# Optimization experiments

Measured on AMD Instinct MI355X. Metric: run time of the kernel, lower is better.

Reference implementation:

```python
import jax, jax.numpy as jnp
import numpy as np

B, P, E, D, A, M, V, L = 128, 196, 2048, 512, 512, 512, 10000, 21


def setup_inputs() -> dict:
    key = jax.random.key(0)
    ks = jax.random.split(key, 24)
    s = 0.02
    encoder_out = jax.random.normal(ks[0], (B, P, E), jnp.float32)
    encoded_captions = jax.random.randint(ks[1], (B, L), 0, V)
    caption_lengths = jax.random.randint(ks[2], (B,), 2, L + 1).at[0].set(L)
    return {
        "encoder_out": encoder_out,
        "encoded_captions": encoded_captions,
        "caption_lengths": caption_lengths,
        "emb_table": jax.random.normal(ks[3], (V, M), jnp.float32) * s,
        "enc_att_w": jax.random.normal(ks[4], (E, A), jnp.float32) * s,
        "enc_att_b": jnp.zeros((A,), jnp.float32),
        "dec_att_w": jax.random.normal(ks[5], (D, A), jnp.float32) * s,
        "dec_att_b": jnp.zeros((A,), jnp.float32),
        "full_att_w": jax.random.normal(ks[6], (A,), jnp.float32) * s,
        "full_att_b": jnp.zeros((), jnp.float32),
        "init_h_w": jax.random.normal(ks[7], (E, D), jnp.float32) * s,
        "init_h_b": jnp.zeros((D,), jnp.float32),
        "init_c_w": jax.random.normal(ks[8], (E, D), jnp.float32) * s,
        "init_c_b": jnp.zeros((D,), jnp.float32),
        "f_beta_w": jax.random.normal(ks[9], (D, E), jnp.float32) * s,
        "f_beta_b": jnp.zeros((E,), jnp.float32),
        "lstm_w_ih": jax.random.normal(ks[10], (4 * D, M + E), jnp.float32) * s,
        "lstm_b_ih": jnp.zeros((4 * D,), jnp.float32),
        "lstm_w_hh": jax.random.normal(ks[11], (4 * D, D), jnp.float32) * s,
        "lstm_b_hh": jnp.zeros((4 * D,), jnp.float32),
        "fc_w": jax.random.normal(ks[12], (V, D), jnp.float32) * s,
        "fc_b": jnp.zeros((V,), jnp.float32),
    }


def reference(encoder_out, encoded_captions, caption_lengths, emb_table,
              enc_att_w, enc_att_b, dec_att_w, dec_att_b, full_att_w, full_att_b,
              init_h_w, init_h_b, init_c_w, init_c_b, f_beta_w, f_beta_b,
              lstm_w_ih, lstm_b_ih, lstm_w_hh, lstm_b_hh, fc_w, fc_b):
    # sort by caption length descending (as in torch)
    order = jnp.argsort(-caption_lengths)
    enc = encoder_out[order]                 # [B,P,E]
    caps = encoded_captions[order]           # [B,L]
    dec_len = caption_lengths[order] - 1     # [B]
    T = caps.shape[1] - 1

    emb_seq = emb_table[caps]                # [B,L,M]
    mean = enc.mean(axis=1)                  # [B,E]
    h0 = mean @ init_h_w + init_h_b
    c0 = mean @ init_c_w + init_c_b
    att1 = enc @ enc_att_w + enc_att_b       # [B,P,A] (hoisted: constant over t)

    def step(carry, t):
        h, c = carry
        att2 = h @ dec_att_w + dec_att_b                              # [B,A]
        e = jnp.einsum('bpa,a->bp', jax.nn.relu(att1 + att2[:, None, :]), full_att_w) + full_att_b
        alpha = jax.nn.softmax(e, axis=1)                             # [B,P]
        awe = jnp.einsum('bpe,bp->be', enc, alpha)                    # [B,E]
        gate = jax.nn.sigmoid(h @ f_beta_w + f_beta_b)                # [B,E]
        x = jnp.concatenate([emb_seq[:, t, :], gate * awe], axis=1)   # [B,M+E]
        g = x @ lstm_w_ih.T + lstm_b_ih + h @ lstm_w_hh.T + lstm_b_hh
        i, f, gg, o = jnp.split(g, 4, axis=1)
        c_new = jax.nn.sigmoid(f) * c + jax.nn.sigmoid(i) * jnp.tanh(gg)
        h_new = jax.nn.sigmoid(o) * jnp.tanh(c_new)
        pred = h_new @ fc_w.T + fc_b                                  # [B,V]
        active = (t < dec_len)[:, None]
        pred = jnp.where(active, pred, 0.0)
        alpha = jnp.where(active, alpha, 0.0)
        return (h_new, c_new), (pred, alpha)

    _, (preds, alphas) = jax.lax.scan(step, (h0, c0), jnp.arange(T))
    predictions = jnp.moveaxis(preds, 0, 1)   # [B,T,V]
    alphas = jnp.moveaxis(alphas, 0, 1)       # [B,T,P]
    return predictions, alphas
```

## Files before the change

kernel.cpp:

```cpp
#include <hip/hip_runtime.h>
#include <math.h>

#define B_ 128
#define P_ 196
#define E_ 2048
#define D_ 512
#define A_ 512
#define M_ 512
#define V_ 10000
#define L_ 21
#define T_ 20

#define NBLK_ 256
#define SLOTS_WORDS (NBLK_ * 16 + 16)

typedef __attribute__((ext_vector_type(8))) short bf16x8;
typedef __attribute__((ext_vector_type(4))) float f32x4;
typedef unsigned short ushort_t;

__global__ void order_kernel(const int* __restrict__ lens, const int* __restrict__ caps,
                             int* __restrict__ order, int* __restrict__ declen,
                             int* __restrict__ row_map, int* __restrict__ tok_rows,
                             unsigned* __restrict__ bar) {
  __shared__ int s_order[B_];
  int tid = threadIdx.x;
  for (int i = tid; i < SLOTS_WORDS; i += 256) bar[i] = 0u;
  if (tid < B_) {
    int li = lens[tid];
    int r = 0;
    for (int j = 0; j < B_; ++j) {
      int lj = lens[j];
      r += (lj > li) || (lj == li && j < tid);
    }
    s_order[r] = tid;
    declen[r] = li - 1;
  }
  __syncthreads();
  if (tid < B_) order[tid] = s_order[tid];
  for (int m = tid; m < B_ * P_; m += blockDim.x) {
    int b = m / P_, p = m - b * P_;
    row_map[m] = s_order[b] * P_ + p;
  }
  for (int i = tid; i < T_ * B_; i += blockDim.x) {
    int t = i >> 7, b = i & 127;
    tok_rows[i] = caps[s_order[b] * L_ + t];
  }
}

__global__ void mean_kernel(const float* __restrict__ enc, const int* __restrict__ order,
                            float* __restrict__ mean) {
  int b = blockIdx.y;
  int e = blockIdx.x * blockDim.x + threadIdx.x;
  int ob = order[b];
  const float* base = enc + (long long)ob * P_ * E_ + e;
  float s = 0.f;
  for (int p = 0; p < P_; ++p) s += base[(long long)p * E_];
  mean[b * E_ + e] = s * (1.0f / P_);
}

__device__ __forceinline__ unsigned f2bf_u(float f) {
  unsigned u = __float_as_uint(f);
  return (u + 0x7fffu + ((u >> 16) & 1u)) >> 16;
}
__device__ __forceinline__ float bf2f(ushort_t h) {
  return __uint_as_float(((unsigned)h) << 16);
}

__global__ void enc2bf_kernel(const float* __restrict__ enc, const int* __restrict__ row_map,
                              ushort_t* __restrict__ out) {
  int r = blockIdx.x;
  int row = row_map[r];
  const float* src = enc + (long long)row * E_ + threadIdx.x * 8;
  float4 v0 = ((const float4*)src)[0];
  float4 v1 = ((const float4*)src)[1];
  float f[8] = {v0.x, v0.y, v0.z, v0.w, v1.x, v1.y, v1.z, v1.w};
  unsigned h[8];
#pragma unroll
  for (int j = 0; j < 8; ++j) h[j] = f2bf_u(f[j]);
  int4 o;
  o.x = (int)(h[0] | (h[1] << 16));
  o.y = (int)(h[2] | (h[3] << 16));
  o.z = (int)(h[4] | (h[5] << 16));
  o.w = (int)(h[6] | (h[7] << 16));
  *(int4*)(out + (long long)r * E_ + threadIdx.x * 8) = o;
}

__global__ void transpose_kernel(const float* __restrict__ in, float* __restrict__ out,
                                 int K, int N) {
  __shared__ float tt[32][33];
  int bx = blockIdx.x * 32;
  int by = blockIdx.y * 32;
  int lx = threadIdx.x & 31, ly = threadIdx.x >> 5;
#pragma unroll
  for (int i = 0; i < 32; i += 8) tt[ly + i][lx] = in[(long long)(by + ly + i) * N + bx + lx];
  __syncthreads();
#pragma unroll
  for (int i = 0; i < 32; i += 8)
    out[(long long)(bx + ly + i) * K + by + lx] = tt[lx][ly + i];
}

__global__ __launch_bounds__(256) void gemm32_kernel(
    const float* __restrict__ A, const float* __restrict__ Bm,
    const float* __restrict__ bias, float* __restrict__ C, int M, int N, int K) {
  __shared__ float As[16][64];
  __shared__ float Bs[16][64];
  const int tid = threadIdx.x;
  const int bm = blockIdx.y * 64, bn = blockIdx.x * 64;
  const int tm = tid >> 4, tn = tid & 15;
  float acc[4][4];
#pragma unroll
  for (int i = 0; i < 4; ++i)
#pragma unroll
    for (int j = 0; j < 4; ++j) acc[i][j] = 0.f;
  const int lm = tid >> 2;
  const int lk = (tid & 3) * 4;
  for (int k0 = 0; k0 < K; k0 += 16) {
    {
      int m = bm + lm;
      float4 v = make_float4(0.f, 0.f, 0.f, 0.f);
      if (m < M) v = *(const float4*)(A + (long long)m * K + k0 + lk);
      As[lk + 0][lm] = v.x;
      As[lk + 1][lm] = v.y;
      As[lk + 2][lm] = v.z;
      As[lk + 3][lm] = v.w;
    }
    {
      int k = tid >> 4;
      int n4 = (tid & 15) * 4;
      int n = bn + n4;
      float4 v = make_float4(0.f, 0.f, 0.f, 0.f);
      if (n < N) v = *(const float4*)(Bm + (long long)(k0 + k) * N + n);
      Bs[k][n4 + 0] = v.x;
      Bs[k][n4 + 1] = v.y;
      Bs[k][n4 + 2] = v.z;
      Bs[k][n4 + 3] = v.w;
    }
    __syncthreads();
#pragma unroll
    for (int k = 0; k < 16; ++k) {
      float a0 = As[k][tm * 4 + 0], a1 = As[k][tm * 4 + 1];
      float a2 = As[k][tm * 4 + 2], a3 = As[k][tm * 4 + 3];
      float b0 = Bs[k][tn * 4 + 0], b1 = Bs[k][tn * 4 + 1];
      float b2 = Bs[k][tn * 4 + 2], b3 = Bs[k][tn * 4 + 3];
      acc[0][0] += a0 * b0; acc[0][1] += a0 * b1; acc[0][2] += a0 * b2; acc[0][3] += a0 * b3;
      acc[1][0] += a1 * b0; acc[1][1] += a1 * b1; acc[1][2] += a1 * b2; acc[1][3] += a1 * b3;
      acc[2][0] += a2 * b0; acc[2][1] += a2 * b1; acc[2][2] += a2 * b2; acc[2][3] += a2 * b3;
      acc[3][0] += a3 * b0; acc[3][1] += a3 * b1; acc[3][2] += a3 * b2; acc[3][3] += a3 * b3;
    }
    __syncthreads();
  }
#pragma unroll
  for (int i = 0; i < 4; ++i) {
    int m = bm + tm * 4 + i;
    if (m >= M) continue;
#pragma unroll
    for (int j = 0; j < 4; ++j) {
      int n = bn + tn * 4 + j;
      if (n >= N) continue;
      C[(long long)m * N + n] = acc[i][j] + (bias ? bias[n] : 0.f);
    }
  }
}

__device__ __forceinline__ void stage16(short* __restrict__ Ph, short* __restrict__ Pl,
                                        int r, int kq, float4 v0, float4 v1, float4 v2,
                                        float4 v3, bool split) {
  float f[16] = {v0.x, v0.y, v0.z, v0.w, v1.x, v1.y, v1.z, v1.w,
                 v2.x, v2.y, v2.z, v2.w, v3.x, v3.y, v3.z, v3.w};
#pragma unroll
  for (int g2 = 0; g2 < 2; ++g2) {
    int gg = (kq >> 3) + g2;
    int slot = gg ^ ((r >> 1) & 3);
    unsigned hb[8];
    float lf[8];
#pragma unroll
    for (int j = 0; j < 8; ++j) {
      float x = f[g2 * 8 + j];
      hb[j] = f2bf_u(x);
      lf[j] = x - __uint_as_float(hb[j] << 16);
    }
    int4 ph;
    ph.x = (int)(hb[0] | (hb[1] << 16));
    ph.y = (int)(hb[2] | (hb[3] << 16));
    ph.z = (int)(hb[4] | (hb[5] << 16));
    ph.w = (int)(hb[6] | (hb[7] << 16));
    *(int4*)&Ph[r * 32 + slot * 8] = ph;
    if (split) {
      unsigned lb[8];
#pragma unroll
      for (int j = 0; j < 8; ++j) lb[j] = f2bf_u(lf[j]);
      int4 pl;
      pl.x = (int)(lb[0] | (lb[1] << 16));
      pl.y = (int)(lb[2] | (lb[3] << 16));
      pl.z = (int)(lb[4] | (lb[5] << 16));
      pl.w = (int)(lb[6] | (lb[7] << 16));
      *(int4*)&Pl[r * 32 + slot * 8] = pl;
    }
  }
}

__device__ __forceinline__ void stage8(short* __restrict__ Ph, short* __restrict__ Pl,
                                       int r, int kq8, float4 v0, float4 v1) {
  int slot = kq8 ^ ((r >> 1) & 3);
  float f[8] = {v0.x, v0.y, v0.z, v0.w, v1.x, v1.y, v1.z, v1.w};
  unsigned hb[8];
  float lf[8];
#pragma unroll
  for (int j = 0; j < 8; ++j) {
    hb[j] = f2bf_u(f[j]);
    lf[j] = f[j] - __uint_as_float(hb[j] << 16);
  }
  int4 ph;
  ph.x = (int)(hb[0] | (hb[1] << 16));
  ph.y = (int)(hb[2] | (hb[3] << 16));
  ph.z = (int)(hb[4] | (hb[5] << 16));
  ph.w = (int)(hb[6] | (hb[7] << 16));
  *(int4*)&Ph[r * 32 + slot * 8] = ph;
  unsigned lb[8];
#pragma unroll
  for (int j = 0; j < 8; ++j) lb[j] = f2bf_u(lf[j]);
  int4 pl;
  pl.x = (int)(lb[0] | (lb[1] << 16));
  pl.y = (int)(lb[2] | (lb[3] << 16));
  pl.z = (int)(lb[4] | (lb[5] << 16));
  pl.w = (int)(lb[6] | (lb[7] << 16));
  *(int4*)&Pl[r * 32 + slot * 8] = pl;
}

__device__ __forceinline__ bf16x8 frag_load(const short* __restrict__ P, int row, int g) {
  int slot = g ^ ((row >> 1) & 3);
  return *(const bf16x8*)&P[row * 32 + slot * 8];
}

template <int MODE, bool SPLIT, bool SWZ, bool OB>
__global__ __launch_bounds__(256) void mfma_gemm(
    const float* __restrict__ A, int lda, const int* __restrict__ row_map,
    const float* __restrict__ Bn, int ldb,
    const float* __restrict__ bias, const float* __restrict__ bias2,
    void* __restrict__ Cv, int ldc, int M, int N, int K,
    const int* __restrict__ declen) {
  __shared__ short Ah[128 * 32];
  __shared__ short Bh[128 * 32];
  __shared__ short Al[128 * 32];
  __shared__ short Bl[128 * 32];
  const int tid = threadIdx.x;
  int bxi, byi;
  if (SWZ) {
    int gx = gridDim.x, gy = gridDim.y;
    int id = blockIdx.y * gx + blockIdx.x;
    int super = 8 * gx;
    int body = (gy & ~7) * gx;
    if (id < body) {
      int s = id / super, rem = id % super;
      byi = s * 8 + (rem & 7);
      bxi = rem >> 3;
    } else {
      int rem = id - body;
      byi = (gy & ~7) + rem / gx;
      bxi = rem % gx;
    }
  } else {
    bxi = blockIdx.x;
    byi = blockIdx.y;
  }
  const int bm = byi * 128, bn = bxi * 128;

  f32x4 acc[4][4];
#pragma unroll
  for (int i = 0; i < 4; ++i)
#pragma unroll
    for (int j = 0; j < 4; ++j) acc[i][j] = (f32x4){0.f, 0.f, 0.f, 0.f};

  const int r = tid >> 1;
  const int kq = (tid & 1) * 16;
  const int am = bm + r;
  const long long arow = row_map ? (long long)row_map[am] : (long long)am;
  const float* ap = A + arow * (long long)lda + kq;
  const int gn = bn + r;
  const float* bp = Bn + (long long)gn * ldb + kq;
  const bool bok = gn < N;

  const int lane = tid & 63;
  const int wv = tid >> 6, wr = wv >> 1, wc = wv & 1;
  const int lr = lane & 15, g = lane >> 4;

  float4 z4 = make_float4(0.f, 0.f, 0.f, 0.f);
  float4 a0 = *(const float4*)(ap), a1 = *(const float4*)(ap + 4);
  float4 a2 = *(const float4*)(ap + 8), a3 = *(const float4*)(ap + 12);
  float4 b0 = bok ? *(const float4*)(bp) : z4;
  float4 b1 = bok ? *(const float4*)(bp + 4) : z4;
  float4 b2 = bok ? *(const float4*)(bp + 8) : z4;
  float4 b3 = bok ? *(const float4*)(bp + 12) : z4;

  for (int k0 = 0; k0 < K; k0 += 32) {
    stage16(Ah, Al, r, kq, a0, a1, a2, a3, SPLIT);
    stage16(Bh, Bl, r, kq, b0, b1, b2, b3, SPLIT);
    __syncthreads();
    if (k0 + 32 < K) {
      int kn = k0 + 32;
      a0 = *(const float4*)(ap + kn);
      a1 = *(const float4*)(ap + kn + 4);
      a2 = *(const float4*)(ap + kn + 8);
      a3 = *(const float4*)(ap + kn + 12);
      b0 = bok ? *(const float4*)(bp + kn) : z4;
      b1 = bok ? *(const float4*)(bp + kn + 4) : z4;
      b2 = bok ? *(const float4*)(bp + kn + 8) : z4;
      b3 = bok ? *(const float4*)(bp + kn + 12) : z4;
    }
    bf16x8 ah[4], bh[4];
#pragma unroll
    for (int i = 0; i < 4; ++i) {
      ah[i] = frag_load(Ah, wr * 64 + i * 16 + lr, g);
      bh[i] = frag_load(Bh, wc * 64 + i * 16 + lr, g);
    }
#pragma unroll
    for (int i = 0; i < 4; ++i)
#pragma unroll
      for (int j = 0; j < 4; ++j)
        acc[i][j] = __builtin_amdgcn_mfma_f32_16x16x32_bf16(ah[i], bh[j], acc[i][j], 0, 0, 0);
    if (SPLIT) {
      bf16x8 al2[4], bl2[4];
#pragma unroll
      for (int i = 0; i < 4; ++i) {
        al2[i] = frag_load(Al, wr * 64 + i * 16 + lr, g);
        bl2[i] = frag_load(Bl, wc * 64 + i * 16 + lr, g);
      }
#pragma unroll
      for (int i = 0; i < 4; ++i)
#pragma unroll
        for (int j = 0; j < 4; ++j)
          acc[i][j] = __builtin_amdgcn_mfma_f32_16x16x32_bf16(al2[i], bh[j], acc[i][j], 0, 0, 0);
#pragma unroll
      for (int i = 0; i < 4; ++i)
#pragma unroll
        for (int j = 0; j < 4; ++j)
          acc[i][j] = __builtin_amdgcn_mfma_f32_16x16x32_bf16(ah[i], bl2[j], acc[i][j], 0, 0, 0);
    }
    __syncthreads();
  }

#pragma unroll
  for (int j = 0; j < 4; ++j) {
    int n = bn + wc * 64 + j * 16 + lr;
    float bj = 0.f;
    if (n < N) {
      if (bias) bj += bias[n];
      if (bias2) bj += bias2[n];
    }
#pragma unroll
    for (int i = 0; i < 4; ++i) {
#pragma unroll
      for (int rr = 0; rr < 4; ++rr) {
        int m = bm + wr * 64 + i * 16 + g * 4 + rr;
        float v = acc[i][j][rr] + bj;
        if (MODE == 0) {
          if (OB)
            ((ushort_t*)Cv)[(long long)m * ldc + n] = (ushort_t)f2bf_u(v);
          else
            ((float*)Cv)[(long long)m * ldc + n] = v;
        } else {
          if (n < N) {
            int b = m & 127, t = m >> 7;
            ((float*)Cv)[(long long)b * (T_ * V_) + (long long)t * V_ + n] =
                (t < declen[b]) ? v : 0.f;
          }
        }
      }
    }
  }
}

__device__ __forceinline__ void mfma_tile64(
    const float* __restrict__ ap, const float* __restrict__ bp, int K,
    f32x4 (&acc)[2][2], short* Ah, short* Al, short* Bh, short* Bl,
    int sr, int skq, int wr, int wc, int lr, int g) {
  float4 a0 = *(const float4*)(ap), a1 = *(const float4*)(ap + 4);
  float4 b0 = *(const float4*)(bp), b1 = *(const float4*)(bp + 4);
  for (int k0 = 0; k0 < K; k0 += 32) {
    stage8(Ah, Al, sr, skq, a0, a1);
    stage8(Bh, Bl, sr, skq, b0, b1);
    __syncthreads();
    if (k0 + 32 < K) {
      a0 = *(const float4*)(ap + k0 + 32);
      a1 = *(const float4*)(ap + k0 + 36);
      b0 = *(const float4*)(bp + k0 + 32);
      b1 = *(const float4*)(bp + k0 + 36);
    }
    bf16x8 fah[2], fbh[2], fal[2], fbl[2];
#pragma unroll
    for (int i = 0; i < 2; ++i) {
      fah[i] = frag_load(Ah, wr * 32 + i * 16 + lr, g);
      fal[i] = frag_load(Al, wr * 32 + i * 16 + lr, g);
      fbh[i] = frag_load(Bh, wc * 32 + i * 16 + lr, g);
      fbl[i] = frag_load(Bl, wc * 32 + i * 16 + lr, g);
    }
#pragma unroll
    for (int i = 0; i < 2; ++i)
#pragma unroll
      for (int j = 0; j < 2; ++j) {
        acc[i][j] = __builtin_amdgcn_mfma_f32_16x16x32_bf16(fah[i], fbh[j], acc[i][j], 0, 0, 0);
        acc[i][j] = __builtin_amdgcn_mfma_f32_16x16x32_bf16(fal[i], fbh[j], acc[i][j], 0, 0, 0);
        acc[i][j] = __builtin_amdgcn_mfma_f32_16x16x32_bf16(fah[i], fbl[j], acc[i][j], 0, 0, 0);
      }
    __syncthreads();
  }
}

__device__ __forceinline__ void gsync(unsigned* __restrict__ slots, unsigned target) {
  __syncthreads();
  if (threadIdx.x == 0) {
    __threadfence();
    __hip_atomic_store(&slots[blockIdx.x * 16], target, __ATOMIC_RELEASE,
                       __HIP_MEMORY_SCOPE_AGENT);
  }
  if (threadIdx.x < 64) {
#pragma unroll
    for (int k = 0; k < 4; ++k) {
      unsigned idx = ((unsigned)threadIdx.x * 4 + k) * 16;
      while (__hip_atomic_load(&slots[idx], __ATOMIC_ACQUIRE, __HIP_MEMORY_SCOPE_AGENT) <
             target) {
        __builtin_amdgcn_s_sleep(2);
      }
    }
    __threadfence();
  }
  __syncthreads();
}

template <bool ENCBF>
__global__ __launch_bounds__(256, 1) void loop_kernel(
    const float* __restrict__ att1f, const ushort_t* __restrict__ att1b,
    const float* __restrict__ encf, const ushort_t* __restrict__ encb,
    const int* __restrict__ order, const int* __restrict__ declen,
    const float* __restrict__ decT, const float* __restrict__ decb,
    const float* __restrict__ fbT, const float* __restrict__ fbb,
    const float* __restrict__ whh, const float* __restrict__ wih,
    const float* __restrict__ faw, const float* __restrict__ fab,
    const float* __restrict__ g_all, float* __restrict__ g_part,
    float* __restrict__ gh, float* __restrict__ h_all, float* __restrict__ c,
    float* __restrict__ xh, float* __restrict__ gate, float* __restrict__ att2,
    float* __restrict__ alphas_out, unsigned* __restrict__ bar) {
  __shared__ short Ah[64 * 32];
  __shared__ short Bh[64 * 32];
  __shared__ short Al[64 * 32];
  __shared__ short Bl[64 * 32];
  __shared__ float att2_s[512];
  __shared__ float w_s[512];
  __shared__ float e_s[P_];
  __shared__ float red[8];

  unsigned* slots = bar;
  unsigned tgt = 0;

  const int bid = blockIdx.x, tid = threadIdx.x;
  const int lane = tid & 63, wv = tid >> 6, wr = wv >> 1, wc = wv & 1;
  const int lr = lane & 15, g = lane >> 4;
  const int sr = tid >> 2, skq = tid & 3;

  const float fb0 = fab[0];
  float wr8[8];
  if (ENCBF) {
    const float4* wp = (const float4*)(faw + lane * 8);
#pragma unroll
    for (int q = 0; q < 2; ++q) {
      float4 v = wp[q];
      wr8[q * 4 + 0] = v.x;
      wr8[q * 4 + 1] = v.y;
      wr8[q * 4 + 2] = v.z;
      wr8[q * 4 + 3] = v.w;
    }
  }

  for (int t = 0; t < T_; ++t) {
    const float* h_cur = h_all + t * (B_ * D_);
    if (bid < 144) {
      int nt = bid % 72, mt = bid / 72;
      int bn = nt * 64;
      const float* Bb;
      if (bn < 512) Bb = decT + bn * 512;
      else if (bn < 2560) Bb = fbT + (bn - 512) * 512;
      else Bb = whh + (bn - 2560) * 512;
      f32x4 acc[2][2];
#pragma unroll
      for (int i = 0; i < 2; ++i)
#pragma unroll
        for (int j = 0; j < 2; ++j) acc[i][j] = (f32x4){0.f, 0.f, 0.f, 0.f};
      mfma_tile64(h_cur + (mt * 64 + sr) * 512 + skq * 8, Bb + sr * 512 + skq * 8, 512,
                  acc, Ah, Al, Bh, Bl, sr, skq, wr, wc, lr, g);
#pragma unroll
      for (int j = 0; j < 2; ++j) {
        int n = bn + wc * 32 + j * 16 + lr;
#pragma unroll
        for (int i = 0; i < 2; ++i) {
#pragma unroll
          for (int rr = 0; rr < 4; ++rr) {
            int m = mt * 64 + wr * 32 + i * 16 + g * 4 + rr;
            float v = acc[i][j][rr];
            if (bn < 512) {
              att2[m * 512 + n] = v + decb[n];
            } else if (bn < 2560) {
              int nc = n - 512;
              gate[m * 2048 + nc] = 1.f / (1.f + __expf(-(v + fbb[nc])));
            } else {
              gh[m * 2048 + (n - 2560)] = v;
            }
          }
        }
      }
    }
    gsync(slots, ++tgt);
    {
      const int b = bid & 127, half = bid >> 7;
      if (ENCBF) {
        float a2r[8];
        const float4* a2p = (const float4*)(att2 + b * 512 + lane * 8);
#pragma unroll
        for (int q = 0; q < 2; ++q) {
          float4 v = a2p[q];
          a2r[q * 4 + 0] = v.x;
          a2r[q * 4 + 1] = v.y;
          a2r[q * 4 + 2] = v.z;
          a2r[q * 4 + 3] = v.w;
        }
        for (int p = wv; p < P_; p += 4) {
          const ushort_t* row = att1b + ((long long)(b * P_ + p)) * 512 + lane * 8;
          bf16x8 hv = *(const bf16x8*)row;
          float s = 0.f;
#pragma unroll
          for (int j = 0; j < 8; ++j) {
            float x = bf2f((ushort_t)hv[j]) + a2r[j];
            s += (x > 0.f ? x : 0.f) * wr8[j];
          }
          for (int off = 32; off; off >>= 1) s += __shfl_down(s, off);
          if (lane == 0) e_s[p] = s + fb0;
        }
      } else {
        for (int i = tid; i < 512; i += 256) {
          att2_s[i] = att2[b * 512 + i];
          w_s[i] = faw[i];
        }
        __syncthreads();
        for (int p = wv; p < P_; p += 4) {
          const float* row = att1f + ((long long)b * P_ + p) * 512;
          float s = 0.f;
#pragma unroll
          for (int i2 = 0; i2 < 8; ++i2) {
            int ix = lane + i2 * 64;
            float v = row[ix] + att2_s[ix];
            s += (v > 0.f ? v : 0.f) * w_s[ix];
          }
          for (int off = 32; off; off >>= 1) s += __shfl_down(s, off);
          if (lane == 0) e_s[p] = s + fb0;
        }
      }
      __syncthreads();
      float mx = -1e30f;
      for (int p = tid; p < P_; p += 256) mx = fmaxf(mx, e_s[p]);
      for (int off = 32; off; off >>= 1) mx = fmaxf(mx, __shfl_down(mx, off));
      if (lane == 0) red[wv] = mx;
      __syncthreads();
      mx = fmaxf(fmaxf(red[0], red[1]), fmaxf(red[2], red[3]));
      float ssum = 0.f;
      for (int p = tid; p < P_; p += 256) {
        float ev = __expf(e_s[p] - mx);
        e_s[p] = ev;
        ssum += ev;
      }
      for (int off = 32; off; off >>= 1) ssum += __shfl_down(ssum, off);
      if (lane == 0) red[4 + wv] = ssum;
      __syncthreads();
      float inv = 1.f / (red[4] + red[5] + red[6] + red[7]);
      const bool active = (t < declen[b]);
      for (int p = tid; p < P_; p += 256) {
        float al = e_s[p] * inv;
        e_s[p] = al;
        if (half == 0)
          alphas_out[(long long)b * (T_ * P_) + t * P_ + p] = active ? al : 0.f;
      }
      __syncthreads();
      if (ENCBF) {
        const ushort_t* eb = encb + (long long)b * (P_ * E_);
        int col = half * 1024 + tid * 4;
        float s0 = 0.f, s1 = 0.f, s2 = 0.f, s3 = 0.f;
#pragma unroll 8
        for (int p = 0; p < P_; ++p) {
          short4 hv = *(const short4*)(eb + (long long)p * E_ + col);
          float a = e_s[p];
          s0 += a * bf2f((ushort_t)hv.x);
          s1 += a * bf2f((ushort_t)hv.y);
          s2 += a * bf2f((ushort_t)hv.z);
          s3 += a * bf2f((ushort_t)hv.w);
        }
        float4 gv = *(const float4*)(gate + b * 2048 + col);
        float4 o;
        o.x = gv.x * s0;
        o.y = gv.y * s1;
        o.z = gv.z * s2;
        o.w = gv.w * s3;
        *(float4*)(xh + b * 2048 + col) = o;
      } else {
        const int ob = order[b];
        const float* eb = encf + (long long)ob * (P_ * E_);
        for (int e0 = half * 1024 + tid; e0 < half * 1024 + 1024; e0 += 256) {
          float s2 = 0.f;
#pragma unroll 4
          for (int p = 0; p < P_; ++p) s2 += e_s[p] * eb[p * 2048 + e0];
          xh[b * 2048 + e0] = gate[b * 2048 + e0] * s2;
        }
      }
    }
    gsync(slots, ++tgt);
    {
      int kc = bid >> 6, rem = bid & 63, mt = rem >> 5, nt = rem & 31;
      int bn = nt * 64;
      f32x4 acc[2][2];
#pragma unroll
      for (int i = 0; i < 2; ++i)
#pragma unroll
        for (int j = 0; j < 2; ++j) acc[i][j] = (f32x4){0.f, 0.f, 0.f, 0.f};
      mfma_tile64(xh + (mt * 64 + sr) * 2048 + kc * 512 + skq * 8,
                  wih + (long long)(bn + sr) * 2560 + 512 + kc * 512 + skq * 8, 512,
                  acc, Ah, Al, Bh, Bl, sr, skq, wr, wc, lr, g);
      float* gp = g_part + kc * (128 * 2048);
#pragma unroll
      for (int j = 0; j < 2; ++j) {
        int n = bn + wc * 32 + j * 16 + lr;
#pragma unroll
        for (int i = 0; i < 2; ++i) {
#pragma unroll
          for (int rr = 0; rr < 4; ++rr) {
            int m = mt * 64 + wr * 32 + i * 16 + g * 4 + rr;
            gp[m * 2048 + n] = acc[i][j][rr];
          }
        }
      }
    }
    gsync(slots, ++tgt);
    {
      int idx = bid * 256 + tid;
      int b = idx >> 9, d = idx & 511;
      int base = b * 2048 + d;
      const float* ge = g_all + (long long)t * (128 * 2048);
      float gi = ge[base] + gh[base];
      float gf2 = ge[base + 512] + gh[base + 512];
      float gg2 = ge[base + 1024] + gh[base + 1024];
      float go = ge[base + 1536] + gh[base + 1536];
#pragma unroll
      for (int kc = 0; kc < 4; ++kc) {
        const float* gp = g_part + kc * (128 * 2048) + base;
        gi += gp[0];
        gf2 += gp[512];
        gg2 += gp[1024];
        go += gp[1536];
      }
      float si = 1.f / (1.f + __expf(-gi));
      float sf = 1.f / (1.f + __expf(-gf2));
      float so = 1.f / (1.f + __expf(-go));
      float cn = sf * c[idx] + si * tanhf(gg2);
      float hn = so * tanhf(cn);
      c[idx] = cn;
      h_all[(t + 1) * (B_ * D_) + idx] = hn;
    }
    gsync(slots, ++tgt);
  }
}

extern "C" void kernel_launch(void* const* d_in, const int* in_sizes, int n_in,
                              void* d_out, int out_size, void* d_ws, size_t ws_size,
                              hipStream_t stream) {
  const float* enc       = (const float*)d_in[0];
  const int*   caps      = (const int*)d_in[1];
  const int*   lens      = (const int*)d_in[2];
  const float* emb       = (const float*)d_in[3];
  const float* enc_att_w = (const float*)d_in[4];
  const float* enc_att_b = (const float*)d_in[5];
  const float* dec_att_w = (const float*)d_in[6];
  const float* dec_att_b = (const float*)d_in[7];
  const float* full_att_w = (const float*)d_in[8];
  const float* full_att_b = (const float*)d_in[9];
  const float* init_h_w  = (const float*)d_in[10];
  const float* init_h_b  = (const float*)d_in[11];
  const float* init_c_w  = (const float*)d_in[12];
  const float* init_c_b  = (const float*)d_in[13];
  const float* f_beta_w  = (const float*)d_in[14];
  const float* f_beta_b  = (const float*)d_in[15];
  const float* lstm_w_ih = (const float*)d_in[16];
  const float* lstm_b_ih = (const float*)d_in[17];
  const float* lstm_w_hh = (const float*)d_in[18];
  const float* lstm_b_hh = (const float*)d_in[19];
  const float* fc_w      = (const float*)d_in[20];
  const float* fc_b      = (const float*)d_in[21];

  float* out = (float*)d_out;
  float* alphas_out = out + (long long)B_ * T_ * V_;

  float* g_all    = out;
  float* g_part   = out + 6 * 1024 * 1024;
  float* encattwT = out + 8 * 1024 * 1024;
  float* decT     = out + 9 * 1024 * 1024 + 512 * 1024;
  float* fbT      = decT + 512 * 512;
  float* gh       = out + 12 * 1024 * 1024;

  size_t cur = 0;
  char* wsb = (char*)d_ws;
  auto alloc = [&](size_t bytes) {
    size_t off = cur;
    cur = (cur + bytes + 255) & ~(size_t)255;
    return (void*)(wsb + off);
  };
  const size_t ATT1B_BYTES = (size_t)B_ * P_ * A_ * 2;
  const size_t ENCB_BYTES  = (size_t)B_ * P_ * E_ * 2;
  const size_t ATT1F_BYTES = (size_t)B_ * P_ * A_ * 4;
  const size_t REST_BYTES  = (size_t)(B_ * E_ + (T_ + 1) * B_ * D_ + B_ * D_ + B_ * A_ +
                                      B_ * E_ + B_ * E_) * 4 +
                             (2 * B_ + B_ * P_ + T_ * B_ + SLOTS_WORDS + 64) * 4 + 4096;
  const bool bfpath = ws_size >= ATT1B_BYTES + ENCB_BYTES + REST_BYTES + (1u << 20);

  ushort_t* att1b = nullptr;
  ushort_t* encbf = nullptr;
  float* att1f = nullptr;
  if (bfpath) {
    att1b = (ushort_t*)alloc(ATT1B_BYTES);
    encbf = (ushort_t*)alloc(ENCB_BYTES);
  } else {
    att1f = (float*)alloc(ATT1F_BYTES);
  }
  float* mean  = (float*)alloc((size_t)B_ * E_ * 4);
  float* h_all = (float*)alloc((size_t)(T_ + 1) * B_ * D_ * 4);
  float* c     = (float*)alloc((size_t)B_ * D_ * 4);
  float* att2  = (float*)alloc((size_t)B_ * A_ * 4);
  float* gate  = (float*)alloc((size_t)B_ * E_ * 4);
  float* xh    = (float*)alloc((size_t)B_ * E_ * 4);
  int* order   = (int*)alloc(B_ * 4);
  int* declen  = (int*)alloc(B_ * 4);
  int* row_map = (int*)alloc((size_t)B_ * P_ * 4);
  int* tok_rows = (int*)alloc((size_t)T_ * B_ * 4);
  unsigned* bar = (unsigned*)alloc(SLOTS_WORDS * 4);

  hipLaunchKernelGGL(order_kernel, dim3(1), dim3(256), 0, stream, lens, caps, order, declen,
                     row_map, tok_rows, bar);
  hipLaunchKernelGGL(transpose_kernel, dim3(16, 64), dim3(256), 0, stream, enc_att_w,
                     encattwT, E_, A_);
  hipLaunchKernelGGL(transpose_kernel, dim3(16, 16), dim3(256), 0, stream, dec_att_w, decT,
                     D_, A_);
  hipLaunchKernelGGL(transpose_kernel, dim3(64, 16), dim3(256), 0, stream, f_beta_w, fbT,
                     D_, E_);
  hipLaunchKernelGGL(mean_kernel, dim3(E_ / 256, B_), dim3(256), 0, stream, enc, order, mean);
  hipLaunchKernelGGL(gemm32_kernel, dim3(D_ / 64, 2), dim3(256), 0, stream, mean, init_h_w,
                     init_h_b, h_all, B_, D_, E_);
  hipLaunchKernelGGL(gemm32_kernel, dim3(D_ / 64, 2), dim3(256), 0, stream, mean, init_c_w,
                     init_c_b, c, B_, D_, E_);
  if (bfpath) {
    hipLaunchKernelGGL((mfma_gemm<0, false, true, true>), dim3(A_ / 128, (B_ * P_) / 128),
                       dim3(256), 0, stream, enc, E_, row_map, encattwT, E_, enc_att_b,
                       (const float*)nullptr, (void*)att1b, A_, B_ * P_, A_, E_,
                       (const int*)nullptr);
    hipLaunchKernelGGL(enc2bf_kernel, dim3(B_ * P_), dim3(256), 0, stream, enc, row_map,
                       encbf);
  } else {
    hipLaunchKernelGGL((mfma_gemm<0, false, true, false>), dim3(A_ / 128, (B_ * P_) / 128),
                       dim3(256), 0, stream, enc, E_, row_map, encattwT, E_, enc_att_b,
                       (const float*)nullptr, (void*)att1f, A_, B_ * P_, A_, E_,
                       (const int*)nullptr);
  }
  hipLaunchKernelGGL((mfma_gemm<0, true, false, false>), dim3((4 * D_) / 128, (T_ * B_) / 128),
                     dim3(256), 0, stream, emb, M_, tok_rows, lstm_w_ih, M_ + E_, lstm_b_ih,
                     lstm_b_hh, (void*)g_all, 4 * D_, T_ * B_, 4 * D_, M_,
                     (const int*)nullptr);
  if (bfpath) {
    hipLaunchKernelGGL((loop_kernel<true>), dim3(NBLK_), dim3(256), 0, stream,
                       (const float*)nullptr, att1b, (const float*)nullptr, encbf, order,
                       declen, decT, dec_att_b, fbT, f_beta_b, lstm_w_hh, lstm_w_ih,
                       full_att_w, full_att_b, g_all, g_part, gh, h_all, c, xh, gate, att2,
                       alphas_out, bar);
  } else {
    hipLaunchKernelGGL((loop_kernel<false>), dim3(NBLK_), dim3(256), 0, stream, att1f,
                       (const ushort_t*)nullptr, enc, (const ushort_t*)nullptr, order,
                       declen, decT, dec_att_b, fbT, f_beta_b, lstm_w_hh, lstm_w_ih,
                       full_att_w, full_att_b, g_all, g_part, gh, h_all, c, xh, gate, att2,
                       alphas_out, bar);
  }
  hipLaunchKernelGGL((mfma_gemm<1, true, false, false>), dim3((V_ + 127) / 128,
                     (T_ * B_) / 128), dim3(256), 0, stream, h_all + B_ * D_, D_,
                     (const int*)nullptr, fc_w, D_, fc_b, (const float*)nullptr, (void*)out,
                     V_, T_ * B_, V_, D_, declen);
}
```

Measured before the change: 5.493 ms.

## Split attention score computation across block pairs and widen weighted-sum loads

In the bf16 path each batch row is handled by two blocks. Before, both blocks computed all 196 attention scores, duplicating the work. Now each block computes half of the scores with batched 8-row loads, publishes them to global memory, and exchanges them with its partner block through a pairwise acquire/release flag spin. The weighted encoder sum now uses 8-wide bf16 loads with a register prefetch pipeline, and the thread groups split the P dimension in halves, combining their partial sums through shared memory. This adds a partner synchronisation per step and a global round trip for scores, in return for halving the redundant score work and improving memory-level parallelism.

Result: faster. 5.261 ms (-4.2%).

```diff
diff --git a/kernel.cpp b/kernel.cpp
--- a/kernel.cpp
+++ b/kernel.cpp
@@ -12,7 +12,7 @@
 #define T_ 20
 
 #define NBLK_ 256
-#define SLOTS_WORDS (NBLK_ * 16 + 16)
+#define SLOTS_WORDS (NBLK_ * 16 + NBLK_ * 16 + 16)
 
 typedef __attribute__((ext_vector_type(8))) short bf16x8;
 typedef __attribute__((ext_vector_type(4))) float f32x4;
@@ -439,7 +439,8 @@
     const float* __restrict__ g_all, float* __restrict__ g_part,
     float* __restrict__ gh, float* __restrict__ h_all, float* __restrict__ c,
     float* __restrict__ xh, float* __restrict__ gate, float* __restrict__ att2,
-    float* __restrict__ alphas_out, unsigned* __restrict__ bar) {
+    float* __restrict__ alphas_out, unsigned* __restrict__ bar,
+    float* __restrict__ e_g) {
   __shared__ short Ah[64 * 32];
   __shared__ short Bh[64 * 32];
   __shared__ short Al[64 * 32];
@@ -450,6 +451,7 @@
   __shared__ float red[8];
 
   unsigned* slots = bar;
+  unsigned* pf = bar + NBLK_ * 16;
   unsigned tgt = 0;
 
   const int bid = blockIdx.x, tid = threadIdx.x;
@@ -522,18 +524,61 @@
           a2r[q * 4 + 2] = v.z;
           a2r[q * 4 + 3] = v.w;
         }
-        for (int p = wv; p < P_; p += 4) {
-          const ushort_t* row = att1b + ((long long)(b * P_ + p)) * 512 + lane * 8;
-          bf16x8 hv = *(const bf16x8*)row;
-          float s = 0.f;
-#pragma unroll
-          for (int j = 0; j < 8; ++j) {
-            float x = bf2f((ushort_t)hv[j]) + a2r[j];
-            s += (x > 0.f ? x : 0.f) * wr8[j];
+        const int pbase = half * 98;
+        const ushort_t* a1base = att1b + ((long long)b * P_ + pbase) * 512 + lane * 8;
+        const bf16x8 zv = (bf16x8)(short)0;
+        for (int p0 = wv * 8; p0 < 98; p0 += 32) {
+          bf16x8 hv[8];
+#pragma unroll
+          for (int q = 0; q < 8; ++q) {
+            int p = p0 + q;
+            hv[q] = (p < 98) ? *(const bf16x8*)(a1base + (long long)p * 512) : zv;
           }
-          for (int off = 32; off; off >>= 1) s += __shfl_down(s, off);
-          if (lane == 0) e_s[p] = s + fb0;
-        }
+          float s[8];
+#pragma unroll
+          for (int q = 0; q < 8; ++q) {
+            float sq = 0.f;
+#pragma unroll
+            for (int j = 0; j < 8; ++j) {
+              float x = bf2f((ushort_t)hv[q][j]) + a2r[j];
+              sq += (x > 0.f ? x : 0.f) * wr8[j];
+            }
+            s[q] = sq;
+          }
+#pragma unroll
+          for (int off = 32; off; off >>= 1) {
+#pragma unroll
+            for (int q = 0; q < 8; ++q) s[q] += __shfl_down(s[q], off);
+          }
+          if (lane == 0) {
+#pragma unroll
+            for (int q = 0; q < 8; ++q) {
+              int p = p0 + q;
+              if (p < 98) {
+                float ev = s[q] + fb0;
+                e_s[pbase + p] = ev;
+                e_g[b * 256 + pbase + p] = ev;
+              }
+            }
+          }
+        }
+        __syncthreads();
+        if (tid == 0) {
+          __threadfence();
+          __hip_atomic_store(&pf[bid * 16], t + 1, __ATOMIC_RELEASE,
+                             __HIP_MEMORY_SCOPE_AGENT);
+          while (__hip_atomic_load(&pf[(bid ^ 128) * 16], __ATOMIC_ACQUIRE,
+                                   __HIP_MEMORY_SCOPE_AGENT) < (unsigned)(t + 1)) {
+            __builtin_amdgcn_s_sleep(2);
+          }
+          __threadfence();
+        }
+        __syncthreads();
+        {
+          const int ppart = (1 - half) * 98;
+          for (int i = tid; i < 98; i += 256) e_s[ppart + i] = e_g[b * 256 + ppart + i];
+        }
+        __syncthreads();
       } else {
         for (int i = tid; i < 512; i += 256) {
           att2_s[i] = att2[b * 512 + i];
@@ -552,8 +597,8 @@
           for (int off = 32; off; off >>= 1) s += __shfl_down(s, off);
           if (lane == 0) e_s[p] = s + fb0;
         }
-      }
-      __syncthreads();
+        __syncthreads();
+      }
       float mx = -1e30f;
       for (int p = tid; p < P_; p += 256) mx = fmaxf(mx, e_s[p]);
       for (int off = 32; off; off >>= 1) mx = fmaxf(mx, __shfl_down(mx, off));
@@ -571,33 +616,150 @@
       __syncthreads();
       float inv = 1.f / (red[4] + red[5] + red[6] + red[7]);
       const bool active = (t < declen[b]);
-      for (int p = tid; p < P_; p += 256) {
-        float al = e_s[p] * inv;
-        e_s[p] = al;
-        if (half == 0)
-          alphas_out[(long long)b * (T_ * P_) + t * P_ + p] = active ? al : 0.f;
+      if (ENCBF) {
+        const int pbase = half * 98;
+        for (int p = tid; p < P_; p += 256) {
+          float al = e_s[p] * inv;
+          e_s[p] = al;
+          if (p >= pbase && p < pbase + 98)
+            alphas_out[(long long)b * (T_ * P_) + t * P_ + p] = active ? al : 0.f;
+        }
+      } else {
+        for (int p = tid; p < P_; p += 256) {
+          float al = e_s[p] * inv;
+          e_s[p] = al;
+          if (half == 0)
+            alphas_out[(long long)b * (T_ * P_) + t * P_ + p] = active ? al : 0.f;
+        }
       }
       __syncthreads();
       if (ENCBF) {
-        const ushort_t* eb = encb + (long long)b * (P_ * E_);
-        int col = half * 1024 + tid * 4;
+        const int tg = tid >> 7;
+        const int tc = tid & 127;
+        const int col = half * 1024 + tc * 8;
+        const ushort_t* ebc =
+            encb + (long long)b * (P_ * E_) + (long long)(tg * 98) * E_ + col;
         float s0 = 0.f, s1 = 0.f, s2 = 0.f, s3 = 0.f;
-#pragma unroll 8
-        for (int p = 0; p < P_; ++p) {
-          short4 hv = *(const short4*)(eb + (long long)p * E_ + col);
-          float a = e_s[p];
-          s0 += a * bf2f((ushort_t)hv.x);
-          s1 += a * bf2f((ushort_t)hv.y);
-          s2 += a * bf2f((ushort_t)hv.z);
-          s3 += a * bf2f((ushort_t)hv.w);
-        }
-        float4 gv = *(const float4*)(gate + b * 2048 + col);
-        float4 o;
-        o.x = gv.x * s0;
-        o.y = gv.y * s1;
-        o.z = gv.z * s2;
-        o.w = gv.w * s3;
-        *(float4*)(xh + b * 2048 + col) = o;
+        float s4 = 0.f, s5 = 0.f, s6 = 0.f, s7 = 0.f;
+        bf16x8 bv0, bv1, bv2, bv3, bv4, bv5, bv6;
+        bv0 = *(const bf16x8*)(ebc + 0LL * E_);
+        bv1 = *(const bf16x8*)(ebc + 1LL * E_);
+        bv2 = *(const bf16x8*)(ebc + 2LL * E_);
+        bv3 = *(const bf16x8*)(ebc + 3LL * E_);
+        bv4 = *(const bf16x8*)(ebc + 4LL * E_);
+        bv5 = *(const bf16x8*)(ebc + 5LL * E_);
+        bv6 = *(const bf16x8*)(ebc + 6LL * E_);
+        const float* ea = e_s + tg * 98;
+        for (int p0 = 0; p0 < 91; p0 += 7) {
+          bf16x8 c0 = bv0, c1 = bv1, c2 = bv2, c3 = bv3, c4 = bv4, c5 = bv5, c6 = bv6;
+          const ushort_t* nb = ebc + (long long)(p0 + 7) * E_;
+          bv0 = *(const bf16x8*)(nb + 0LL * E_);
+          bv1 = *(const bf16x8*)(nb + 1LL * E_);
+          bv2 = *(const bf16x8*)(nb + 2LL * E_);
+          bv3 = *(const bf16x8*)(nb + 3LL * E_);
+          bv4 = *(const bf16x8*)(nb + 4LL * E_);
+          bv5 = *(const bf16x8*)(nb + 5LL * E_);
+          bv6 = *(const bf16x8*)(nb + 6LL * E_);
+          float a;
+          a = ea[p0 + 0];
+          s0 += a * bf2f((ushort_t)c0[0]); s1 += a * bf2f((ushort_t)c0[1]);
+          s2 += a * bf2f((ushort_t)c0[2]); s3 += a * bf2f((ushort_t)c0[3]);
+          s4 += a * bf2f((ushort_t)c0[4]); s5 += a * bf2f((ushort_t)c0[5]);
+          s6 += a * bf2f((ushort_t)c0[6]); s7 += a * bf2f((ushort_t)c0[7]);
+          a = ea[p0 + 1];
+          s0 += a * bf2f((ushort_t)c1[0]); s1 += a * bf2f((ushort_t)c1[1]);
+          s2 += a * bf2f((ushort_t)c1[2]); s3 += a * bf2f((ushort_t)c1[3]);
+          s4 += a * bf2f((ushort_t)c1[4]); s5 += a * bf2f((ushort_t)c1[5]);
+          s6 += a * bf2f((ushort_t)c1[6]); s7 += a * bf2f((ushort_t)c1[7]);
+          a = ea[p0 + 2];
+          s0 += a * bf2f((ushort_t)c2[0]); s1 += a * bf2f((ushort_t)c2[1]);
+          s2 += a * bf2f((ushort_t)c2[2]); s3 += a * bf2f((ushort_t)c2[3]);
+          s4 += a * bf2f((ushort_t)c2[4]); s5 += a * bf2f((ushort_t)c2[5]);
+          s6 += a * bf2f((ushort_t)c2[6]); s7 += a * bf2f((ushort_t)c2[7]);
+          a = ea[p0 + 3];
+          s0 += a * bf2f((ushort_t)c3[0]); s1 += a * bf2f((ushort_t)c3[1]);
+          s2 += a * bf2f((ushort_t)c3[2]); s3 += a * bf2f((ushort_t)c3[3]);
+          s4 += a * bf2f((ushort_t)c3[4]); s5 += a * bf2f((ushort_t)c3[5]);
+          s6 += a * bf2f((ushort_t)c3[6]); s7 += a * bf2f((ushort_t)c3[7]);
+          a = ea[p0 + 4];
+          s0 += a * bf2f((ushort_t)c4[0]); s1 += a * bf2f((ushort_t)c4[1]);
+          s2 += a * bf2f((ushort_t)c4[2]); s3 += a * bf2f((ushort_t)c4[3]);
+          s4 += a * bf2f((ushort_t)c4[4]); s5 += a * bf2f((ushort_t)c4[5]);
+          s6 += a * bf2f((ushort_t)c4[6]); s7 += a * bf2f((ushort_t)c4[7]);
+          a = ea[p0 + 5];
+          s0 += a * bf2f((ushort_t)c5[0]); s1 += a * bf2f((ushort_t)c5[1]);
+          s2 += a * bf2f((ushort_t)c5[2]); s3 += a * bf2f((ushort_t)c5[3]);
+          s4 += a * bf2f((ushort_t)c5[4]); s5 += a * bf2f((ushort_t)c5[5]);
+          s6 += a * bf2f((ushort_t)c5[6]); s7 += a * bf2f((ushort_t)c5[7]);
+          a = ea[p0 + 6];
+          s0 += a * bf2f((ushort_t)c6[0]); s1 += a * bf2f((ushort_t)c6[1]);
+          s2 += a * bf2f((ushort_t)c6[2]); s3 += a * bf2f((ushort_t)c6[3]);
+          s4 += a * bf2f((ushort_t)c6[4]); s5 += a * bf2f((ushort_t)c6[5]);
+          s6 += a * bf2f((ushort_t)c6[6]); s7 += a * bf2f((ushort_t)c6[7]);
+        }
+        {
+          float a;
+          a = ea[91];
+          s0 += a * bf2f((ushort_t)bv0[0]); s1 += a * bf2f((ushort_t)bv0[1]);
+          s2 += a * bf2f((ushort_t)bv0[2]); s3 += a * bf2f((ushort_t)bv0[3]);
+          s4 += a * bf2f((ushort_t)bv0[4]); s5 += a * bf2f((ushort_t)bv0[5]);
+          s6 += a * bf2f((ushort_t)bv0[6]); s7 += a * bf2f((ushort_t)bv0[7]);
+          a = ea[92];
+          s0 += a * bf2f((ushort_t)bv1[0]); s1 += a * bf2f((ushort_t)bv1[1]);
+          s2 += a * bf2f((ushort_t)bv1[2]); s3 += a * bf2f((ushort_t)bv1[3]);
+          s4 += a * bf2f((ushort_t)bv1[4]); s5 += a * bf2f((ushort_t)bv1[5]);
+          s6 += a * bf2f((ushort_t)bv1[6]); s7 += a * bf2f((ushort_t)bv1[7]);
+          a = ea[93];
+          s0 += a * bf2f((ushort_t)bv2[0]); s1 += a * bf2f((ushort_t)bv2[1]);
+          s2 += a * bf2f((ushort_t)bv2[2]); s3 += a * bf2f((ushort_t)bv2[3]);
+          s4 += a * bf2f((ushort_t)bv2[4]); s5 += a * bf2f((ushort_t)bv2[5]);
+          s6 += a * bf2f((ushort_t)bv2[6]); s7 += a * bf2f((ushort_t)bv2[7]);
+          a = ea[94];
+          s0 += a * bf2f((ushort_t)bv3[0]); s1 += a * bf2f((ushort_t)bv3[1]);
+          s2 += a * bf2f((ushort_t)bv3[2]); s3 += a * bf2f((ushort_t)bv3[3]);
+          s4 += a * bf2f((ushort_t)bv3[4]); s5 += a * bf2f((ushort_t)bv3[5]);
+          s6 += a * bf2f((ushort_t)bv3[6]); s7 += a * bf2f((ushort_t)bv3[7]);
+          a = ea[95];
+          s0 += a * bf2f((ushort_t)bv4[0]); s1 += a * bf2f((ushort_t)bv4[1]);
+          s2 += a * bf2f((ushort_t)bv4[2]); s3 += a * bf2f((ushort_t)bv4[3]);
+          s4 += a * bf2f((ushort_t)bv4[4]); s5 += a * bf2f((ushort_t)bv4[5]);
+          s6 += a * bf2f((ushort_t)bv4[6]); s7 += a * bf2f((ushort_t)bv4[7]);
+          a = ea[96];
+          s0 += a * bf2f((ushort_t)bv5[0]); s1 += a * bf2f((ushort_t)bv5[1]);
+          s2 += a * bf2f((ushort_t)bv5[2]); s3 += a * bf2f((ushort_t)bv5[3]);
+          s4 += a * bf2f((ushort_t)bv5[4]); s5 += a * bf2f((ushort_t)bv5[5]);
+          s6 += a * bf2f((ushort_t)bv5[6]); s7 += a * bf2f((ushort_t)bv5[7]);
+          a = ea[97];
+          s0 += a * bf2f((ushort_t)bv6[0]); s1 += a * bf2f((ushort_t)bv6[1]);
+          s2 += a * bf2f((ushort_t)bv6[2]); s3 += a * bf2f((ushort_t)bv6[3]);
+          s4 += a * bf2f((ushort_t)bv6[4]); s5 += a * bf2f((ushort_t)bv6[5]);
+          s6 += a * bf2f((ushort_t)bv6[6]); s7 += a * bf2f((ushort_t)bv6[7]);
+        }
+        float* awe_s = (float*)Ah;
+        __syncthreads();
+        if (tg == 1) {
+          awe_s[tc * 8 + 0] = s0; awe_s[tc * 8 + 1] = s1;
+          awe_s[tc * 8 + 2] = s2; awe_s[tc * 8 + 3] = s3;
+          awe_s[tc * 8 + 4] = s4; awe_s[tc * 8 + 5] = s5;
+          awe_s[tc * 8 + 6] = s6; awe_s[tc * 8 + 7] = s7;
+        }
+        __syncthreads();
+        if (tg == 0) {
+          float4 gv0 = *(const float4*)(gate + b * 2048 + col);
+          float4 gv1 = *(const float4*)(gate + b * 2048 + col + 4);
+          float4 o0, o1;
+          o0.x = gv0.x * (s0 + awe_s[tc * 8 + 0]);
+          o0.y = gv0.y * (s1 + awe_s[tc * 8 + 1]);
+          o0.z = gv0.z * (s2 + awe_s[tc * 8 + 2]);
+          o0.w = gv0.w * (s3 + awe_s[tc * 8 + 3]);
+          o1.x = gv1.x * (s4 + awe_s[tc * 8 + 4]);
+          o1.y = gv1.y * (s5 + awe_s[tc * 8 + 5]);
+          o1.z = gv1.z * (s6 + awe_s[tc * 8 + 6]);
+          o1.w = gv1.w * (s7 + awe_s[tc * 8 + 7]);
+          *(float4*)(xh + b * 2048 + col) = o0;
+          *(float4*)(xh + b * 2048 + col + 4) = o1;
+        }
+        __syncthreads();
       } else {
         const int ob = order[b];
         const float* eb = encf + (long long)ob * (P_ * E_);
@@ -700,6 +862,7 @@
   float* decT     = out + 9 * 1024 * 1024 + 512 * 1024;
   float* fbT      = decT + 512 * 512;
   float* gh       = out + 12 * 1024 * 1024;
+  float* e_g      = out + 13 * 1024 * 1024;
 
   size_t cur = 0;
   char* wsb = (char*)d_ws;
@@ -772,13 +935,13 @@
                        (const float*)nullptr, att1b, (const float*)nullptr, encbf, order,
                        declen, decT, dec_att_b, fbT, f_beta_b, lstm_w_hh, lstm_w_ih,
                        full_att_w, full_att_b, g_all, g_part, gh, h_all, c, xh, gate, att2,
-                       alphas_out, bar);
+                       alphas_out, bar, e_g);
   } else {
     hipLaunchKernelGGL((loop_kernel<false>), dim3(NBLK_), dim3(256), 0, stream, att1f,
                        (const ushort_t*)nullptr, enc, (const ushort_t*)nullptr, order,
                        declen, decT, dec_att_b, fbT, f_beta_b, lstm_w_hh, lstm_w_ih,
                        full_att_w, full_att_b, g_all, g_part, gh, h_all, c, xh, gate, att2,
-                       alphas_out, bar);
+                       alphas_out, bar, e_g);
   }
   hipLaunchKernelGGL((mfma_gemm<1, true, false, false>), dim3((V_ + 127) / 128,
                      (T_ * B_) / 128), dim3(256), 0, stream, h_all + B_ * D_, D_,
```
